# Kernel tuning notes

Measured on AMD Instinct MI355X. Metric: run time of the kernel, lower is better.

The kernel has to match this reference:

```python
import jax, jax.numpy as jnp
import numpy as np

T, B, I, H = 512, 64, 256, 256
ACT_EXP2 = 7   # activation scale = 2^-7
W_EXP2 = 8     # weight scale = 2^-8
QMIN, QMAX = -128.0, 127.0  # int8 symmetric, zp=0


def fq(x, exp2_inv):
    """Fake-quantize (round/clamp/dequant) with straight-through estimator."""
    scale = 2.0 ** (-exp2_inv)
    y = jnp.clip(jnp.round(x / scale), QMIN, QMAX) * scale
    return x + jax.lax.stop_gradient(y - x)


def setup_inputs() -> dict:
    key = jax.random.key(0)
    k = jax.random.split(key, 5)
    x = jax.random.normal(k[0], (T, B, I), jnp.float32)
    h0 = jnp.zeros((B, H), jnp.float32)
    W = jax.random.normal(k[1], (I, 3 * H), jnp.float32) / np.sqrt(I)
    R = jax.random.normal(k[2], (H, 3 * H), jnp.float32) / np.sqrt(H)
    bx = jax.random.normal(k[3], (3 * H,), jnp.float32) * 0.1
    br = jax.random.normal(k[4], (3 * H,), jnp.float32) * 0.1
    return {"x": x, "h0": h0, "W": W, "R": R, "bx": bx, "br": br}


def gru_quant(x, h0, W, R, bx, br):
    # quantize weights/biases once (weight.W / weight.R / weight.bx / weight.br)
    Wq = fq(W, W_EXP2)
    Rq = fq(R, W_EXP2)
    bxq = fq(bx, W_EXP2)
    brq = fq(br, W_EXP2)
    # hoisted input matmul: Wx = fq(fq(x) @ Wq)  -> [T, B, 3H]
    Wx = fq(jnp.einsum('tbi,ij->tbj', fq(x, ACT_EXP2), Wq), ACT_EXP2)
    Hh = h0.shape[-1]
    bz, brg, bg = bxq[:Hh], bxq[Hh:2 * Hh], bxq[2 * Hh:]

    def step(h, wx_t):
        hq = fq(h, ACT_EXP2)                      # input.h
        Rh = fq(hq @ Rq, ACT_EXP2)                # matmul.Rh
        v = fq(Rh + brq, ACT_EXP2)                # op.Rh_add_br
        wz, wr, wg = wx_t[:, :Hh], wx_t[:, Hh:2 * Hh], wx_t[:, 2 * Hh:]
        vz, vr, vg = v[:, :Hh], v[:, Hh:2 * Hh], v[:, 2 * Hh:]
        z = fq(jax.nn.sigmoid(fq(wz + bz + vz, ACT_EXP2)), ACT_EXP2)  # gate.z
        r = fq(jax.nn.sigmoid(fq(wr + brg + vr, ACT_EXP2)), ACT_EXP2)  # gate.r
        rRh = fq(r * vg, ACT_EXP2)                # op.rRh
        g = fq(jnp.tanh(fq(wg + bg + rRh, ACT_EXP2)), ACT_EXP2)        # gate.g
        old = fq(z * h, ACT_EXP2)                 # op.old_contrib
        new = fq((1.0 - z) * g, ACT_EXP2)         # op.new_contrib
        h_new = old + new
        return h_new, h_new

    _, hs = jax.lax.scan(step, h0, Wx)  # hs: [T, B, H]
    return hs


def reference(x, h0, W, R, bx, br):
    return gru_quant(x, h0, W, R, bx, br)
```

## Files before the change

### kernel.cpp

```cpp
#include <hip/hip_runtime.h>
#include <hip/hip_bf16.h>
#include <stdint.h>


#define T_STEPS 512
#define BATCH   64
#define IDIM    256
#define HDIM    256
#define N3H     768

#if defined(__has_builtin)
#if __has_builtin(__builtin_amdgcn_sdot4)
#define DOT4(a,b,c) __builtin_amdgcn_sdot4((int)(a),(int)(b),(int)(c),false)
#endif
#endif
#ifndef DOT4
__device__ __forceinline__ int dot4_sw(uint32_t a, uint32_t b, int c){
  c += (int)(int8_t)(a)      * (int)(int8_t)(b);
  c += (int)(int8_t)(a>>8)   * (int)(int8_t)(b>>8);
  c += (int)(int8_t)(a>>16)  * (int)(int8_t)(b>>16);
  c += (int)(int8_t)(a>>24)  * (int)(int8_t)(b>>24);
  return c;
}
#define DOT4(a,b,c) dot4_sw((uint32_t)(a),(uint32_t)(b),(int)(c))
#endif

#define CHUNK(W,c) (((c)&3)==0 ? W[(c)>>2].x : ((c)&3)==1 ? W[(c)>>2].y : \
                    ((c)&3)==2 ? W[(c)>>2].z : W[(c)>>2].w)

__device__ __forceinline__ void barrier_lds() {
  asm volatile("s_waitcnt lgkmcnt(0)\n\ts_barrier" ::: "memory");
}

__device__ __forceinline__ int clamp8(int x)   { return min(127, max(-128, x)); }
__device__ __forceinline__ int rne_half(int y) { int t = y >> 1; return t + (t & y & 1); }
__device__ __forceinline__ int rne_s8(int s)   { return (s + 127 + ((s >> 8) & 1)) >> 8; }
__device__ __forceinline__ int rne_s7(int p)   { return (p + 63 + ((p >> 7) & 1)) >> 7; }

__device__ __forceinline__ int rneclamp(float v) {
  int q = (int)rintf(v);
  return min(127, max(-128, q));
}

__device__ __forceinline__ uint32_t packq4(float4 f, float sc) {
  uint32_t b0 = (uint32_t)(uint8_t)(int8_t)rneclamp(f.x * sc);
  uint32_t b1 = (uint32_t)(uint8_t)(int8_t)rneclamp(f.y * sc);
  uint32_t b2 = (uint32_t)(uint8_t)(int8_t)rneclamp(f.z * sc);
  uint32_t b3 = (uint32_t)(uint8_t)(int8_t)rneclamp(f.w * sc);
  return b0 | (b1 << 8) | (b2 << 16) | (b3 << 24);
}

__global__ void prep_kernel(const float* __restrict__ W, const float* __restrict__ R,
                            const float* __restrict__ bx, const float* __restrict__ br,
                            int8_t* __restrict__ Wq, int8_t* __restrict__ Rq,
                            int8_t* __restrict__ bx8, int8_t* __restrict__ br8) {
  const int NW = IDIM * N3H;
  int idx = blockIdx.x * 256 + threadIdx.x;
  if (idx < NW) {
    int k = idx / N3H, j = idx % N3H;
    Wq[((size_t)(k >> 4) * N3H + j) * 16 + (k & 15)] = (int8_t)rneclamp(W[idx] * 256.0f);
  } else if (idx < 2 * NW) {
    int i2 = idx - NW;
    int k = i2 / N3H, j = i2 % N3H;
    Rq[(size_t)j * HDIM + k] = (int8_t)rneclamp(R[i2] * 256.0f);
  } else if (idx < 2 * NW + N3H) {
    int i2 = idx - 2 * NW;
    bx8[i2] = (int8_t)rneclamp(bx[i2] * 256.0f);
  } else if (idx < 2 * NW + 2 * N3H) {
    int i2 = idx - 2 * NW - N3H;
    br8[i2] = (int8_t)rneclamp(br[i2] * 256.0f);
  }
}

__global__ __launch_bounds__(768, 1) void gemm_wx_kernel(
    const float* __restrict__ x, const int8_t* __restrict__ Wq,
    int8_t* __restrict__ WxQ8) {
  const int t = blockIdx.x;
  const int j = threadIdx.x;

  __shared__ uint4 xq4[64 * 16];
  uint32_t* xq = (uint32_t*)xq4;

  uint4 w[16];
  const uint4* wp = (const uint4*)Wq;
  #pragma unroll
  for (int kk = 0; kk < 16; ++kk) w[kk] = wp[kk * N3H + j];

  const float4* xg = (const float4*)(x) + (size_t)t * 4096;
  for (int i = j; i < 4096; i += 768) {
    float4 f = xg[i];
    xq[i] = packq4(f, 128.0f);
  }
  __syncthreads();

  for (int r = 0; r < 64; ++r) {
    int s = 0;
    #pragma unroll
    for (int kk = 0; kk < 16; ++kk) {
      uint4 hv = xq4[r * 16 + kk];
      s = DOT4(hv.x, w[kk].x, s);
      s = DOT4(hv.y, w[kk].y, s);
      s = DOT4(hv.z, w[kk].z, s);
      s = DOT4(hv.w, w[kk].w, s);
    }
    int q = clamp8(rne_s8(s));
    WxQ8[((size_t)r * T_STEPS + t) * N3H + j] = (int8_t)q;
  }
}

__global__ __launch_bounds__(512) __attribute__((amdgpu_waves_per_eu(2, 2)))
void gru_rec10_kernel(
    const float* __restrict__ h0, const int8_t* __restrict__ Rq,
    const int8_t* __restrict__ bx8, const int8_t* __restrict__ br8,
    const int8_t* __restrict__ WxQ8, float* __restrict__ out) {
  const int b = blockIdx.x;
  const int tid = threadIdx.x;
  const int j = tid & 255;
  const int lane = tid & 63;

  __shared__ uint32_t hq[2][64];
  __shared__ int zirl[256];
  __shared__ int8_t lutS[256];
  __shared__ int8_t lutT[256];

  {
    double a = ((double)j - 128.0) / 128.0;
    if (tid < 256) {
      lutS[j] = (int8_t)min(127, max(-128, (int)rint(128.0 / (1.0 + exp(-a)))));
    } else {
      lutT[j] = (int8_t)min(127, max(-128, (int)rint(128.0 * tanh(a))));
      int h00 = (int)rintf(h0[b * HDIM + j] * 128.0f);
      ((int8_t*)&hq[0][0])[j] = (int8_t)clamp8(h00);
    }
  }
  __syncthreads();

  if (tid < 256) {
    uint4 wz[16], wr[16];
    {
      const uint4* pz = (const uint4*)(Rq + (size_t)j * HDIM);
      const uint4* pr = (const uint4*)(Rq + (size_t)(j + 256) * HDIM);
      #pragma unroll
      for (int kk = 0; kk < 16; ++kk) { wz[kk] = pz[kk]; wr[kk] = pr[kk]; }
    }
    const int bz  = (int)bx8[j];
    const int brg = (int)bx8[j + 256];
    const int vbz = (int)br8[j];
    const int vbr = (int)br8[j + 256];
    const int8_t* wxp = WxQ8 + (size_t)b * T_STEPS * N3H + j;

    int zA = (int)wxp[0],   rA = (int)wxp[256];
    int zB = (int)wxp[N3H], rB = (int)wxp[N3H + 256];

    for (int t = 0; t < T_STEPS; ++t) {
      const int cur = t & 1;
      const int8_t* p = wxp + (size_t)min(t + 2, T_STEPS - 1) * N3H;
      int zn = (int)p[0], rn = (int)p[256];

      uint32_t hw = hq[cur][lane];
      int sz = 0, sr = 0;
      #pragma unroll
      for (int c = 0; c < 64; ++c) {
        int hc = __builtin_amdgcn_readlane((int)hw, c);
        sz = DOT4(hc, CHUNK(wz, c), sz);
        sr = DOT4(hc, CHUNK(wr, c), sr);
      }
      int vz = clamp8(rne_half(2 * clamp8(rne_s8(sz)) + vbz));
      int vr = clamp8(rne_half(2 * clamp8(rne_s8(sr)) + vbr));
      int az = clamp8(rne_half(2 * (zA + vz) + bz));
      int zi = (int)lutS[az + 128];
      int ar = clamp8(rne_half(2 * (rA + vr) + brg));
      int ri = (int)lutS[ar + 128];
      zirl[j] = zi | (ri << 16);

      zA = zB; rA = rB; zB = zn; rB = rn;

      barrier_lds();
      barrier_lds();
    }
  } else {
    uint4 wg[16];
    {
      const uint4* pg = (const uint4*)(Rq + (size_t)(j + 512) * HDIM);
      #pragma unroll
      for (int kk = 0; kk < 16; ++kk) wg[kk] = pg[kk];
    }
    const int bg  = (int)bx8[j + 512];
    const int vbg = (int)br8[j + 512];
    int hi = (int)rintf(h0[b * HDIM + j] * 128.0f);
    const int8_t* wxp = WxQ8 + (size_t)b * T_STEPS * N3H + j + 512;
    float* outp = out + (size_t)b * HDIM + j;

    int gA = (int)wxp[0], gB = (int)wxp[N3H];

    for (int t = 0; t < T_STEPS; ++t) {
      const int cur = t & 1, nxt = cur ^ 1;
      const int8_t* p = wxp + (size_t)min(t + 2, T_STEPS - 1) * N3H;
      int gn = (int)p[0];

      uint32_t hw = hq[cur][lane];
      int sg = 0;
      #pragma unroll
      for (int c = 0; c < 64; ++c) {
        int hc = __builtin_amdgcn_readlane((int)hw, c);
        sg = DOT4(hc, CHUNK(wg, c), sg);
      }
      int vg = clamp8(rne_half(2 * clamp8(rne_s8(sg)) + vbg));

      barrier_lds();
      int zr_ = zirl[j];
      int zi = zr_ & 0xffff;
      int ri = zr_ >> 16;
      int rrh = clamp8(rne_s7(ri * vg));
      int ag = clamp8(rne_half(2 * (gA + rrh) + bg));
      int gi = (int)lutT[ag + 128];
      int oldi = clamp8(rne_s7(zi * hi));
      int newi = clamp8(rne_s7((128 - zi) * gi));
      hi = oldi + newi;
      outp[(size_t)t * BATCH * HDIM] = (float)hi * (1.0f / 128.0f);
      ((int8_t*)&hq[nxt][0])[j] = (int8_t)clamp8(hi);

      gA = gB; gB = gn;

      barrier_lds();
    }
  }
}

extern "C" void kernel_launch(void* const* d_in, const int* in_sizes, int n_in,
                              void* d_out, int out_size, void* d_ws, size_t ws_size,
                              hipStream_t stream) {
  const float* x  = (const float*)d_in[0];
  const float* h0 = (const float*)d_in[1];
  const float* W  = (const float*)d_in[2];
  const float* R  = (const float*)d_in[3];
  const float* bx = (const float*)d_in[4];
  const float* br = (const float*)d_in[5];
  float* out = (float*)d_out;

  const size_t NW = (size_t)IDIM * N3H;
  int8_t* Wq  = (int8_t*)d_ws;
  int8_t* Rq  = Wq + NW;
  int8_t* bx8 = Rq + NW;
  int8_t* br8 = bx8 + N3H;
  int8_t* WxQ8 = br8 + N3H;

  {
    int total = (int)(2 * NW + 2 * N3H);
    int blocks = (total + 255) / 256;
    prep_kernel<<<blocks, 256, 0, stream>>>(W, R, bx, br, Wq, Rq, bx8, br8);
  }
  gemm_wx_kernel<<<T_STEPS, 768, 0, stream>>>(x, Wq, WxQ8);
  gru_rec10_kernel<<<BATCH, 512, 0, stream>>>(h0, Rq, bx8, br8, WxQ8, out);
}
```

Before: 556.4 us.

## Rebalance GRU gate split and reload recurrent weights from cache each step

Repartitions the recurrent kernel so the first 256 threads compute the z and g gates plus the state update, while the other 256 compute only the r gate and publish it through LDS. Rq is re-laid out in 16-byte k-chunks interleaved across columns so loads are coalesced. Recurrent weights are now reloaded from global memory/L2 every timestep instead of staying in registers, and the waves_per_eu hint is dropped, presumably to relieve register pressure. The risk is that per-step global weight reloads sit on the serial critical path and add latency to every one of the 512 steps.

```diff
diff --git a/kernel.cpp b/kernel.cpp
--- a/kernel.cpp
+++ b/kernel.cpp
@@ -62,7 +62,7 @@
   } else if (idx < 2 * NW) {
     int i2 = idx - NW;
     int k = i2 / N3H, j = i2 % N3H;
-    Rq[(size_t)j * HDIM + k] = (int8_t)rneclamp(R[i2] * 256.0f);
+    Rq[((size_t)(k >> 4) * N3H + j) * 16 + (k & 15)] = (int8_t)rneclamp(R[i2] * 256.0f);
   } else if (idx < 2 * NW + N3H) {
     int i2 = idx - 2 * NW;
     bx8[i2] = (int8_t)rneclamp(bx[i2] * 256.0f);
@@ -108,8 +108,8 @@
   }
 }
 
-__global__ __launch_bounds__(512) __attribute__((amdgpu_waves_per_eu(2, 2)))
-void gru_rec10_kernel(
+__global__ __launch_bounds__(512, 1)
+void gru_rec11_kernel(
     const float* __restrict__ h0, const int8_t* __restrict__ Rq,
     const int8_t* __restrict__ bx8, const int8_t* __restrict__ br8,
     const int8_t* __restrict__ WxQ8, float* __restrict__ out) {
@@ -119,109 +119,97 @@
   const int lane = tid & 63;
 
   __shared__ uint32_t hq[2][64];
-  __shared__ int zirl[256];
+  __shared__ int rbuf[256];
   __shared__ int8_t lutS[256];
   __shared__ int8_t lutT[256];
 
-  {
+  const uint4* rp = (const uint4*)Rq;
+
+  int hi = 0;
+  if (tid < 256) {
     double a = ((double)j - 128.0) / 128.0;
-    if (tid < 256) {
-      lutS[j] = (int8_t)min(127, max(-128, (int)rint(128.0 / (1.0 + exp(-a)))));
-    } else {
-      lutT[j] = (int8_t)min(127, max(-128, (int)rint(128.0 * tanh(a))));
-      int h00 = (int)rintf(h0[b * HDIM + j] * 128.0f);
-      ((int8_t*)&hq[0][0])[j] = (int8_t)clamp8(h00);
-    }
+    lutS[j] = (int8_t)min(127, max(-128, (int)rint(128.0 / (1.0 + exp(-a)))));
+    hi = (int)rintf(h0[b * HDIM + j] * 128.0f);
+    ((int8_t*)&hq[0][0])[j] = (int8_t)clamp8(hi);
+  } else {
+    double a = ((double)j - 128.0) / 128.0;
+    lutT[j] = (int8_t)min(127, max(-128, (int)rint(128.0 * tanh(a))));
   }
   __syncthreads();
 
   if (tid < 256) {
-    uint4 wz[16], wr[16];
-    {
-      const uint4* pz = (const uint4*)(Rq + (size_t)j * HDIM);
-      const uint4* pr = (const uint4*)(Rq + (size_t)(j + 256) * HDIM);
-      #pragma unroll
-      for (int kk = 0; kk < 16; ++kk) { wz[kk] = pz[kk]; wr[kk] = pr[kk]; }
-    }
-    const int bz  = (int)bx8[j];
-    const int brg = (int)bx8[j + 256];
+    const int bzc = (int)bx8[j];
     const int vbz = (int)br8[j];
-    const int vbr = (int)br8[j + 256];
+    const int bgc = (int)bx8[j + 512];
+    const int vbg = (int)br8[j + 512];
     const int8_t* wxp = WxQ8 + (size_t)b * T_STEPS * N3H + j;
-
-    int zA = (int)wxp[0],   rA = (int)wxp[256];
-    int zB = (int)wxp[N3H], rB = (int)wxp[N3H + 256];
+    float* outp = out + (size_t)b * HDIM + j;
+    int zA = (int)wxp[0],   gA = (int)wxp[512];
+    int zB = (int)wxp[N3H], gB = (int)wxp[N3H + 512];
 
     for (int t = 0; t < T_STEPS; ++t) {
-      const int cur = t & 1;
+      const int cur = t & 1, nxt = cur ^ 1;
+      uint4 wz[16], wg[16];
+      #pragma unroll
+      for (int kk = 0; kk < 16; ++kk) {
+        wz[kk] = rp[kk * N3H + j];
+        wg[kk] = rp[kk * N3H + 512 + j];
+      }
       const int8_t* p = wxp + (size_t)min(t + 2, T_STEPS - 1) * N3H;
-      int zn = (int)p[0], rn = (int)p[256];
+      int zn = (int)p[0], gn = (int)p[512];
 
       uint32_t hw = hq[cur][lane];
-      int sz = 0, sr = 0;
+      int sz = 0, sg = 0;
       #pragma unroll
       for (int c = 0; c < 64; ++c) {
         int hc = __builtin_amdgcn_readlane((int)hw, c);
         sz = DOT4(hc, CHUNK(wz, c), sz);
-        sr = DOT4(hc, CHUNK(wr, c), sr);
+        sg = DOT4(hc, CHUNK(wg, c), sg);
       }
       int vz = clamp8(rne_half(2 * clamp8(rne_s8(sz)) + vbz));
-      int vr = clamp8(rne_half(2 * clamp8(rne_s8(sr)) + vbr));
-      int az = clamp8(rne_half(2 * (zA + vz) + bz));
+      int vg = clamp8(rne_half(2 * clamp8(rne_s8(sg)) + vbg));
+      int az = clamp8(rne_half(2 * (zA + vz) + bzc));
       int zi = (int)lutS[az + 128];
-      int ar = clamp8(rne_half(2 * (rA + vr) + brg));
-      int ri = (int)lutS[ar + 128];
-      zirl[j] = zi | (ri << 16);
-
-      zA = zB; rA = rB; zB = zn; rB = rn;
-
-      barrier_lds();
-      barrier_lds();
-    }
-  } else {
-    uint4 wg[16];
-    {
-      const uint4* pg = (const uint4*)(Rq + (size_t)(j + 512) * HDIM);
-      #pragma unroll
-      for (int kk = 0; kk < 16; ++kk) wg[kk] = pg[kk];
-    }
-    const int bg  = (int)bx8[j + 512];
-    const int vbg = (int)br8[j + 512];
-    int hi = (int)rintf(h0[b * HDIM + j] * 128.0f);
-    const int8_t* wxp = WxQ8 + (size_t)b * T_STEPS * N3H + j + 512;
-    float* outp = out + (size_t)b * HDIM + j;
-
-    int gA = (int)wxp[0], gB = (int)wxp[N3H];
-
-    for (int t = 0; t < T_STEPS; ++t) {
-      const int cur = t & 1, nxt = cur ^ 1;
-      const int8_t* p = wxp + (size_t)min(t + 2, T_STEPS - 1) * N3H;
-      int gn = (int)p[0];
-
-      uint32_t hw = hq[cur][lane];
-      int sg = 0;
-      #pragma unroll
-      for (int c = 0; c < 64; ++c) {
-        int hc = __builtin_amdgcn_readlane((int)hw, c);
-        sg = DOT4(hc, CHUNK(wg, c), sg);
-      }
-      int vg = clamp8(rne_half(2 * clamp8(rne_s8(sg)) + vbg));
-
-      barrier_lds();
-      int zr_ = zirl[j];
-      int zi = zr_ & 0xffff;
-      int ri = zr_ >> 16;
+
+      barrier_lds();
+      int ri = rbuf[j];
       int rrh = clamp8(rne_s7(ri * vg));
-      int ag = clamp8(rne_half(2 * (gA + rrh) + bg));
+      int ag = clamp8(rne_half(2 * (gA + rrh) + bgc));
       int gi = (int)lutT[ag + 128];
       int oldi = clamp8(rne_s7(zi * hi));
       int newi = clamp8(rne_s7((128 - zi) * gi));
       hi = oldi + newi;
       outp[(size_t)t * BATCH * HDIM] = (float)hi * (1.0f / 128.0f);
       ((int8_t*)&hq[nxt][0])[j] = (int8_t)clamp8(hi);
-
-      gA = gB; gB = gn;
-
+      zA = zB; gA = gB; zB = zn; gB = gn;
+      barrier_lds();
+    }
+  } else {
+    const int brc = (int)bx8[j + 256];
+    const int vbr = (int)br8[j + 256];
+    const int8_t* wxp = WxQ8 + (size_t)b * T_STEPS * N3H + 256 + j;
+    int rA = (int)wxp[0], rB = (int)wxp[N3H];
+
+    for (int t = 0; t < T_STEPS; ++t) {
+      const int cur = t & 1;
+      uint4 wr[16];
+      #pragma unroll
+      for (int kk = 0; kk < 16; ++kk) wr[kk] = rp[kk * N3H + 256 + j];
+      const int8_t* p = wxp + (size_t)min(t + 2, T_STEPS - 1) * N3H;
+      int rn = (int)p[0];
+
+      uint32_t hw = hq[cur][lane];
+      int sr = 0;
+      #pragma unroll
+      for (int c = 0; c < 64; ++c) {
+        int hc = __builtin_amdgcn_readlane((int)hw, c);
+        sr = DOT4(hc, CHUNK(wr, c), sr);
+      }
+      int vr = clamp8(rne_half(2 * clamp8(rne_s8(sr)) + vbr));
+      int ar = clamp8(rne_half(2 * (rA + vr) + brc));
+      rbuf[j] = (int)lutS[ar + 128];
+      rA = rB; rB = rn;
+      barrier_lds();
       barrier_lds();
     }
   }
@@ -251,5 +239,5 @@
     prep_kernel<<<blocks, 256, 0, stream>>>(W, R, bx, br, Wq, Rq, bx8, br8);
   }
   gemm_wx_kernel<<<T_STEPS, 768, 0, stream>>>(x, Wq, WxQ8);
-  gru_rec10_kernel<<<BATCH, 512, 0, stream>>>(h0, Rq, bx8, br8, WxQ8, out);
-}
+  gru_rec11_kernel<<<BATCH, 512, 0, stream>>>(h0, Rq, bx8, br8, WxQ8, out);
+}
```

Result: no change. 563.2 us (+1.2%).
